# Optimization experiments

Hardware: AMD Instinct MI355X
Metric: run time of the kernel (lower is better)

## Reference

```python
import jax, jax.numpy as jnp
import numpy as np

B, T, V = 32, 100, 20000
E, H, M, DD = 128, 128, 64, 2


def setup_inputs() -> dict:
    key = jax.random.key(0)
    ks = jax.random.split(key, 12)
    x = jax.random.uniform(ks[0], (B, T, V), dtype=jnp.float32)
    # zero out trailing timesteps per example so Masking layer matters
    lens = jax.random.randint(ks[1], (B,), T * 3 // 4, T + 1)
    tmask = (jnp.arange(T)[None, :] < lens[:, None]).astype(jnp.float32)
    x = x * tmask[:, :, None]
    a = jax.random.uniform(ks[2], (B, V), dtype=jnp.float32)
    d = jax.random.normal(ks[3], (B, DD), dtype=jnp.float32)
    # parameters
    emb = jax.random.uniform(ks[4], (V, E), minval=-0.1, maxval=0.1, dtype=jnp.float32)
    s = 1.0 / np.sqrt(E)
    gru_k = jax.random.uniform(ks[5], (E, 3 * H), minval=-s, maxval=s, dtype=jnp.float32)
    gru_rk = jax.random.normal(ks[6], (H, 3 * H), dtype=jnp.float32) / np.sqrt(H)
    gru_b_i = jnp.zeros((3 * H,), jnp.float32)   # input bias (reset_after=True)
    gru_b_r = jnp.zeros((3 * H,), jnp.float32)   # recurrent bias
    s1 = 1.0 / np.sqrt(H + E)
    W1 = jax.random.uniform(ks[7], (H + E, M), minval=-s1, maxval=s1, dtype=jnp.float32)
    b1 = jnp.zeros((M,), jnp.float32)
    s2 = 1.0 / np.sqrt(M + DD)
    W2 = jax.random.uniform(ks[8], (M + DD, 1), minval=-s2, maxval=s2, dtype=jnp.float32)
    b2 = jnp.zeros((1,), jnp.float32)
    return dict(x=x, a=a, d=d, emb=emb, gru_k=gru_k, gru_rk=gru_rk,
                gru_b_i=gru_b_i, gru_b_r=gru_b_r, W1=W1, b1=b1, W2=W2, b2=b2)


def _gru_final_state(xe, mask, gru_k, gru_rk, gru_b_i, gru_b_r):
    # xe: [B,T,E], mask: [B,T] bool. Keras GRU, reset_after=True, eval mode (dropout off).
    Hn = gru_rk.shape[0]
    x_proj = jnp.einsum('bte,eh->bth', xe, gru_k) + gru_b_i  # [B,T,3H]

    def step(h, inp):
        xp_t, m_t = inp                      # [B,3H], [B]
        rec = h @ gru_rk + gru_b_r           # [B,3H]
        xz, xr, xh = jnp.split(xp_t, 3, axis=-1)
        rz, rr, rh = jnp.split(rec, 3, axis=-1)
        z = jax.nn.sigmoid(xz + rz)
        r = jax.nn.sigmoid(xr + rr)
        hh = jnp.tanh(xh + r * rh)
        h_new = z * h + (1.0 - z) * hh
        h = jnp.where(m_t[:, None], h_new, h)  # masked steps carry state
        return h, None

    h0 = jnp.zeros((xe.shape[0], Hn), xe.dtype)
    h_final, _ = jax.lax.scan(step, h0, (jnp.swapaxes(x_proj, 0, 1), jnp.swapaxes(mask, 0, 1)))
    return h_final


def reference(x, a, d, emb, gru_k, gru_rk, gru_b_i, gru_b_r, W1, b1, W2, b2):
    ae = jnp.tanh(a @ emb)                       # [B,E]
    xe = jnp.tanh(jnp.einsum('btv,ve->bte', x, emb))  # [B,T,E]
    mask = jnp.any(xe != 0.0, axis=-1)           # Masking(mask_value=0.0)
    h = _gru_final_state(xe, mask, gru_k, gru_rk, gru_b_i, gru_b_r)  # [B,H]
    c = jnp.tanh(jnp.concatenate([h, ae], axis=1) @ W1 + b1)         # [B,M]
    out = jax.nn.sigmoid(jnp.concatenate([c, d], axis=1) @ W2 + b2)  # [B,1]
    return out
```

## Files before the change

### kernel.cpp

```cpp
#include <hip/hip_runtime.h>

typedef __attribute__((ext_vector_type(8))) short short8;
typedef __attribute__((ext_vector_type(4))) float float4v;

#define V_ 20000

__device__ __forceinline__ unsigned short f2bf(float f) {
    union { float f; unsigned int u; } v; v.f = f;
    unsigned int u = v.u;
    u += 0x7fffu + ((u >> 16) & 1u);
    return (unsigned short)(u >> 16);
}

__device__ __forceinline__ float fast_tanh(float x) {
    float xc = fminf(15.f, fmaxf(-15.f, x));
    float e = __expf(2.f * xc);
    return (e - 1.f) / (e + 1.f);
}

__device__ __forceinline__ float sigmoidf_(float x) {
    float xc = fminf(30.f, fmaxf(-30.f, x));
    return 1.f / (1.f + __expf(-xc));
}

#define GLL16(gp, lp) __builtin_amdgcn_global_load_lds( \
    (const __attribute__((address_space(1))) void*)(gp), \
    (__attribute__((address_space(3))) void*)(lp), 16, 0, 0)

__global__ __launch_bounds__(256) void cvt_embT(const float* __restrict__ emb,
                                                unsigned short* __restrict__ embT) {
    __shared__ unsigned short tile[128 * 65];
    int tid = threadIdx.x;
    int k0 = blockIdx.x * 64;
    const float4v* e4 = (const float4v*)emb;
    #pragma unroll
    for (int c = 0; c < 8; ++c) {
        int l4 = c * 256 + tid;
        int k = l4 >> 5;
        int n4 = l4 & 31;
        float4v f = {0.f, 0.f, 0.f, 0.f};
        if (k0 + k < V_) f = e4[(size_t)(k0 + k) * 32 + n4];
        tile[(n4 * 4 + 0) * 65 + k] = f2bf(f.x);
        tile[(n4 * 4 + 1) * 65 + k] = f2bf(f.y);
        tile[(n4 * 4 + 2) * 65 + k] = f2bf(f.z);
        tile[(n4 * 4 + 3) * 65 + k] = f2bf(f.w);
    }
    __syncthreads();
    #pragma unroll
    for (int c = 0; c < 4; ++c) {
        int l8 = c * 256 + tid;
        int n = l8 >> 3, seg = l8 & 7;
        int kk = k0 + seg * 8;
        if (kk < V_) {
            short8 v;
            #pragma unroll
            for (int i = 0; i < 8; ++i) v[i] = (short)tile[n * 65 + seg * 8 + i];
            *(short8*)(embT + (size_t)n * V_ + kk) = v;
        }
    }
}

__global__ __launch_bounds__(256, 4) void big_gemm(const float* __restrict__ x,
                                                   const float* __restrict__ a,
                                                   const unsigned short* __restrict__ embT,
                                                   float* __restrict__ partial,
                                                   int ks) {
    __shared__ unsigned short Alds[2][128 * 40];
    __shared__ unsigned short Blds[2][128 * 32];
    int tid = threadIdx.x;
    int bx = blockIdx.x, by = blockIdx.y;
    int m0 = bx * 128;
    int per = 625 / ks, extra = 625 % ks;
    int kb0 = by * per + (by < extra ? by : extra);
    int nkb = per + (by < extra ? 1 : 0);

    int lane = tid & 63, wave = tid >> 6;
    int wr = wave >> 1, wc = wave & 1;
    int ln = lane & 15, quad = lane >> 4;

    float4v acc[4][4];
    #pragma unroll
    for (int i = 0; i < 4; ++i)
        #pragma unroll
        for (int j = 0; j < 4; ++j) acc[i][j] = (float4v){0.f, 0.f, 0.f, 0.f};

    int row = tid >> 1, seg = tid & 1;
    int rg = m0 + row;
    int aidx = rg - 3200; aidx = aidx < 0 ? 0 : (aidx > 31 ? 31 : aidx);
    const float* __restrict__ srcA = (rg < 3200) ? (x + (size_t)rg * V_)
                                                 : (a + (size_t)aidx * V_);
    int brow0 = tid >> 2, bkq = tid & 3;
    int wbase = tid & ~63;
    const unsigned short* gB0 = embT + (size_t)brow0 * V_ + bkq * 8;
    const unsigned short* gB1 = embT + (size_t)(64 + brow0) * V_ + bkq * 8;

    float4v fa0, fa1, fa2, fa3;

    {
        int k0 = kb0 * 32;
        const float4v* ap = (const float4v*)(srcA + k0 + seg * 16);
        fa0 = ap[0]; fa1 = ap[1]; fa2 = ap[2]; fa3 = ap[3];
        GLL16(gB0 + k0, &Blds[0][(size_t)wbase * 8]);
        GLL16(gB1 + k0, &Blds[0][(size_t)(256 + wbase) * 8]);
        short8 w0, w1;
        w0[0]=(short)f2bf(fa0.x); w0[1]=(short)f2bf(fa0.y); w0[2]=(short)f2bf(fa0.z); w0[3]=(short)f2bf(fa0.w);
        w0[4]=(short)f2bf(fa1.x); w0[5]=(short)f2bf(fa1.y); w0[6]=(short)f2bf(fa1.z); w0[7]=(short)f2bf(fa1.w);
        w1[0]=(short)f2bf(fa2.x); w1[1]=(short)f2bf(fa2.y); w1[2]=(short)f2bf(fa2.z); w1[3]=(short)f2bf(fa2.w);
        w1[4]=(short)f2bf(fa3.x); w1[5]=(short)f2bf(fa3.y); w1[6]=(short)f2bf(fa3.z); w1[7]=(short)f2bf(fa3.w);
        *(short8*)&Alds[0][row * 40 + seg * 16]     = w0;
        *(short8*)&Alds[0][row * 40 + seg * 16 + 8] = w1;
    }
    __syncthreads();

    for (int it = 0; it < nkb; ++it) {
        int buf = it & 1, nxt = buf ^ 1;
        bool more = (it + 1 < nkb);
        if (more) {
            int k0 = (kb0 + it + 1) * 32;
            const float4v* ap = (const float4v*)(srcA + k0 + seg * 16);
            fa0 = ap[0]; fa1 = ap[1]; fa2 = ap[2]; fa3 = ap[3];
            GLL16(gB0 + k0, &Blds[nxt][(size_t)wbase * 8]);
            GLL16(gB1 + k0, &Blds[nxt][(size_t)(256 + wbase) * 8]);
        }
        short8 af[4];
        #pragma unroll
        for (int i = 0; i < 4; ++i)
            af[i] = *(const short8*)&Alds[buf][(wr * 64 + i * 16 + ln) * 40 + quad * 8];
        #pragma unroll
        for (int j = 0; j < 4; ++j) {
            short8 bf = *(const short8*)&Blds[buf][(wc * 64 + j * 16 + ln) * 32 + quad * 8];
            #pragma unroll
            for (int i = 0; i < 4; ++i)
                acc[i][j] = __builtin_amdgcn_mfma_f32_16x16x32_bf16(af[i], bf, acc[i][j], 0, 0, 0);
        }
        if (more) {
            short8 w0, w1;
            w0[0]=(short)f2bf(fa0.x); w0[1]=(short)f2bf(fa0.y); w0[2]=(short)f2bf(fa0.z); w0[3]=(short)f2bf(fa0.w);
            w0[4]=(short)f2bf(fa1.x); w0[5]=(short)f2bf(fa1.y); w0[6]=(short)f2bf(fa1.z); w0[7]=(short)f2bf(fa1.w);
            w1[0]=(short)f2bf(fa2.x); w1[1]=(short)f2bf(fa2.y); w1[2]=(short)f2bf(fa2.z); w1[3]=(short)f2bf(fa2.w);
            w1[4]=(short)f2bf(fa3.x); w1[5]=(short)f2bf(fa3.y); w1[6]=(short)f2bf(fa3.z); w1[7]=(short)f2bf(fa3.w);
            *(short8*)&Alds[nxt][row * 40 + seg * 16]     = w0;
            *(short8*)&Alds[nxt][row * 40 + seg * 16 + 8] = w1;
        }
        __syncthreads();
    }

    float* dst = partial + (size_t)by * 3328 * 128;
    #pragma unroll
    for (int i = 0; i < 4; ++i) {
        #pragma unroll
        for (int j = 0; j < 4; ++j) {
            int rowb = m0 + wr * 64 + i * 16 + quad * 4;
            int col = wc * 64 + j * 16 + ln;
            #pragma unroll
            for (int r = 0; r < 4; ++r)
                dst[(size_t)(rowb + r) * 128 + col] = acc[i][j][r];
        }
    }
}

__global__ __launch_bounds__(384) void xproj_fused(const float* __restrict__ partial,
                                                   const float* __restrict__ gru_k,
                                                   const float* __restrict__ b_i,
                                                   float* __restrict__ xproj,
                                                   float* __restrict__ maskg,
                                                   float* __restrict__ ae,
                                                   int ks) {
    const size_t SL = (size_t)3328 * 128;
    int tid = threadIdx.x;
    if (blockIdx.x == 200) {
        for (int i = tid; i < 32 * 128; i += 384) {
            float s = 0.f;
            for (int k = 0; k < ks; ++k) s += partial[(size_t)k * SL + 3200 * 128 + i];
            ae[i] = fast_tanh(s);
        }
        return;
    }
    __shared__ float xs[16 * 128];
    __shared__ int anyr[16];
    int row0 = blockIdx.x * 16;
    if (tid < 16) anyr[tid] = 0;
    __syncthreads();
    const float4v* p4 = (const float4v*)partial + (size_t)row0 * 32;
    const size_t SL4 = SL / 4;
    for (int i4 = tid; i4 < 512; i4 += 384) {
        float4v s = p4[i4];
        for (int k = 1; k < ks; ++k) {
            float4v t = p4[(size_t)k * SL4 + i4];
            s.x += t.x; s.y += t.y; s.z += t.z; s.w += t.w;
        }
        float4v v;
        v.x = fast_tanh(s.x); v.y = fast_tanh(s.y);
        v.z = fast_tanh(s.z); v.w = fast_tanh(s.w);
        *(float4v*)&xs[i4 * 4] = v;
        if (v.x != 0.f || v.y != 0.f || v.z != 0.f || v.w != 0.f)
            anyr[i4 >> 5] = 1;
    }
    __syncthreads();
    if (tid < 16) maskg[row0 + tid] = anyr[tid] ? 1.f : 0.f;

    int j = tid;
    float acc[16];
    #pragma unroll
    for (int r = 0; r < 16; ++r) acc[r] = 0.f;
    float bi = b_i[j];
    for (int k4 = 0; k4 < 32; ++k4) {
        float g0 = gru_k[(k4 * 4 + 0) * 384 + j];
        float g1 = gru_k[(k4 * 4 + 1) * 384 + j];
        float g2 = gru_k[(k4 * 4 + 2) * 384 + j];
        float g3 = gru_k[(k4 * 4 + 3) * 384 + j];
        #pragma unroll
        for (int r = 0; r < 16; ++r) {
            float4v xv = *(const float4v*)&xs[r * 128 + k4 * 4];
            acc[r] = fmaf(xv.x, g0, acc[r]);
            acc[r] = fmaf(xv.y, g1, acc[r]);
            acc[r] = fmaf(xv.z, g2, acc[r]);
            acc[r] = fmaf(xv.w, g3, acc[r]);
        }
    }
    #pragma unroll
    for (int r = 0; r < 16; ++r)
        xproj[(size_t)(row0 + r) * 384 + j] = acc[r] + bi;
}

__global__ __launch_bounds__(384) void gru_fused(const float* __restrict__ xproj,
                                                 const float* __restrict__ maskg,
                                                 const float* __restrict__ gru_rk,
                                                 const float* __restrict__ b_r,
                                                 const float* __restrict__ ae,
                                                 const float* __restrict__ d,
                                                 const float* __restrict__ W1,
                                                 const float* __restrict__ b1,
                                                 const float* __restrict__ W2,
                                                 const float* __restrict__ b2,
                                                 float* __restrict__ out) {
    int b = blockIdx.x;
    int j = threadIdx.x;
    float w[128];
    #pragma unroll
    for (int k = 0; k < 128; ++k) w[k] = gru_rk[k * 384 + j];
    float br = b_r[j];
    __shared__ float4v hs4[32];
    __shared__ float recs[384];
    float* hs = (float*)hs4;
    float hreg = 0.f;
    if (j < 128) hs[j] = 0.f;
    const float* xp_base = xproj + (size_t)b * 100 * 384;
    const float* mk = maskg + b * 100;
    float xz = 0.f, xr = 0.f, xh = 0.f;
    if (j < 128) { xz = xp_base[j]; xr = xp_base[128 + j]; xh = xp_base[256 + j]; }
    __syncthreads();
    for (int t = 0; t < 100; ++t) {
        float nxz = 0.f, nxr = 0.f, nxh = 0.f;
        if (t < 99 && j < 128) {
            const float* nb = xp_base + (t + 1) * 384;
            nxz = nb[j]; nxr = nb[128 + j]; nxh = nb[256 + j];
        }
        float s0 = 0.f, s1 = 0.f, s2 = 0.f, s3 = 0.f;
        #pragma unroll
        for (int k4 = 0; k4 < 32; ++k4) {
            float4v hv = hs4[k4];
            s0 = fmaf(hv.x, w[k4 * 4 + 0], s0);
            s1 = fmaf(hv.y, w[k4 * 4 + 1], s1);
            s2 = fmaf(hv.z, w[k4 * 4 + 2], s2);
            s3 = fmaf(hv.w, w[k4 * 4 + 3], s3);
        }
        recs[j] = br + ((s0 + s1) + (s2 + s3));
        __syncthreads();
        if (j < 128) {
            float z = sigmoidf_(xz + recs[j]);
            float r = sigmoidf_(xr + recs[128 + j]);
            float hh = fast_tanh(xh + r * recs[256 + j]);
            float hn = z * hreg + (1.f - z) * hh;
            hreg = (mk[t] != 0.f) ? hn : hreg;
            hs[j] = hreg;
        }
        __syncthreads();
        xz = nxz; xr = nxr; xh = nxh;
    }
    if (j < 64) {
        int m = j;
        float s = b1[m];
        const float* ab = ae + b * 128;
        #pragma unroll 4
        for (int k = 0; k < 128; ++k) s = fmaf(hs[k], W1[k * 64 + m], s);
        #pragma unroll 4
        for (int k = 0; k < 128; ++k) s = fmaf(ab[k], W1[(128 + k) * 64 + m], s);
        float c = fast_tanh(s);
        float p = c * W2[m];
        #pragma unroll
        for (int off = 32; off > 0; off >>= 1) p += __shfl_down(p, off);
        if (m == 0) {
            p += d[b * 2 + 0] * W2[64] + d[b * 2 + 1] * W2[65] + b2[0];
            out[b] = sigmoidf_(p);
        }
    }
}

extern "C" void kernel_launch(void* const* d_in, const int* in_sizes, int n_in,
                              void* d_out, int out_size, void* d_ws, size_t ws_size,
                              hipStream_t stream) {
    (void)in_sizes; (void)n_in; (void)out_size;
    const float* x      = (const float*)d_in[0];
    const float* a      = (const float*)d_in[1];
    const float* d      = (const float*)d_in[2];
    const float* emb    = (const float*)d_in[3];
    const float* gru_k  = (const float*)d_in[4];
    const float* gru_rk = (const float*)d_in[5];
    const float* gbi    = (const float*)d_in[6];
    const float* gbr    = (const float*)d_in[7];
    const float* W1     = (const float*)d_in[8];
    const float* b1     = (const float*)d_in[9];
    const float* W2     = (const float*)d_in[10];
    const float* b2     = (const float*)d_in[11];
    float* out = (float*)d_out;

    char* ws = (char*)d_ws;
    unsigned short* embT = (unsigned short*)(ws);
    const size_t slice = (size_t)3328 * 128 * 4;
    float* partial = (float*)(ws + 5120000);

    int ks = 16;
    {
        size_t fixed_rest = 16384 + 12800 + 4915200;
        while (ks > 1 && 5120000 + (size_t)ks * slice + fixed_rest > ws_size) ks >>= 1;
    }
    char* after = ws + 5120000 + (size_t)ks * slice;
    float* ae      = (float*)(after);
    float* maskg   = (float*)(after + 16384);
    float* xproj   = (float*)(after + 29184);

    hipLaunchKernelGGL(cvt_embT,    dim3(313),    dim3(256), 0, stream, emb, embT);
    hipLaunchKernelGGL(big_gemm,    dim3(26, ks), dim3(256), 0, stream, x, a, embT, partial, ks);
    hipLaunchKernelGGL(xproj_fused, dim3(201),    dim3(384), 0, stream, partial, gru_k, gbi, xproj, maskg, ae, ks);
    hipLaunchKernelGGL(gru_fused,   dim3(32),     dim3(384), 0, stream, xproj, maskg, gru_rk, gbr,
                       ae, d, W1, b1, W2, b2, out);
}
```

Before: 564.9 us.

## Use packed FP32 FMA in projection and GRU, skip trailing masked steps

Rewrites the input-projection and recurrent matvec inner loops to use 2-wide float vectors with elementwise FMA, so the compiler can emit packed FP32 FMA instructions (v_pk_fma_f32) and halve the instruction count. The GRU kernel also computes the last valid timestep per batch from the mask with a shared atomicMax and runs the recurrence only up to that point. Trailing masked steps only carry state, so skipping them is exact, but interior masked steps are still executed. The packed form changes the accumulation order slightly.

```diff
diff --git a/kernel.cpp b/kernel.cpp
--- a/kernel.cpp
+++ b/kernel.cpp
@@ -2,6 +2,7 @@
 
 typedef __attribute__((ext_vector_type(8))) short short8;
 typedef __attribute__((ext_vector_type(4))) float float4v;
+typedef __attribute__((ext_vector_type(2))) float float2v;
 
 #define V_ 20000
 
@@ -200,27 +201,24 @@
     if (tid < 16) maskg[row0 + tid] = anyr[tid] ? 1.f : 0.f;
 
     int j = tid;
-    float acc[16];
-    #pragma unroll
-    for (int r = 0; r < 16; ++r) acc[r] = 0.f;
+    float2v acc[16];
+    #pragma unroll
+    for (int r = 0; r < 16; ++r) acc[r] = (float2v){0.f, 0.f};
     float bi = b_i[j];
     for (int k4 = 0; k4 < 32; ++k4) {
-        float g0 = gru_k[(k4 * 4 + 0) * 384 + j];
-        float g1 = gru_k[(k4 * 4 + 1) * 384 + j];
-        float g2 = gru_k[(k4 * 4 + 2) * 384 + j];
-        float g3 = gru_k[(k4 * 4 + 3) * 384 + j];
+        float2v g01 = { gru_k[(k4 * 4 + 0) * 384 + j], gru_k[(k4 * 4 + 1) * 384 + j] };
+        float2v g23 = { gru_k[(k4 * 4 + 2) * 384 + j], gru_k[(k4 * 4 + 3) * 384 + j] };
         #pragma unroll
         for (int r = 0; r < 16; ++r) {
             float4v xv = *(const float4v*)&xs[r * 128 + k4 * 4];
-            acc[r] = fmaf(xv.x, g0, acc[r]);
-            acc[r] = fmaf(xv.y, g1, acc[r]);
-            acc[r] = fmaf(xv.z, g2, acc[r]);
-            acc[r] = fmaf(xv.w, g3, acc[r]);
+            float2v x01 = {xv.x, xv.y}, x23 = {xv.z, xv.w};
+            acc[r] = __builtin_elementwise_fma(x01, g01, acc[r]);
+            acc[r] = __builtin_elementwise_fma(x23, g23, acc[r]);
         }
     }
     #pragma unroll
     for (int r = 0; r < 16; ++r)
-        xproj[(size_t)(row0 + r) * 384 + j] = acc[r] + bi;
+        xproj[(size_t)(row0 + r) * 384 + j] = (acc[r].x + acc[r].y) + bi;
 }
 
 __global__ __launch_bounds__(384) void gru_fused(const float* __restrict__ xproj,
@@ -236,36 +234,45 @@
                                                  float* __restrict__ out) {
     int b = blockIdx.x;
     int j = threadIdx.x;
-    float w[128];
-    #pragma unroll
-    for (int k = 0; k < 128; ++k) w[k] = gru_rk[k * 384 + j];
+    float2v wv[64];
+    #pragma unroll
+    for (int i = 0; i < 64; ++i) {
+        wv[i] = (float2v){ gru_rk[(2 * i) * 384 + j], gru_rk[(2 * i + 1) * 384 + j] };
+    }
     float br = b_r[j];
     __shared__ float4v hs4[32];
     __shared__ float recs[384];
+    __shared__ int ntS;
     float* hs = (float*)hs4;
     float hreg = 0.f;
+    if (j == 0) ntS = 0;
     if (j < 128) hs[j] = 0.f;
     const float* xp_base = xproj + (size_t)b * 100 * 384;
     const float* mk = maskg + b * 100;
     float xz = 0.f, xr = 0.f, xh = 0.f;
     if (j < 128) { xz = xp_base[j]; xr = xp_base[128 + j]; xh = xp_base[256 + j]; }
     __syncthreads();
-    for (int t = 0; t < 100; ++t) {
+    if (j < 100 && mk[j] != 0.f) atomicMax(&ntS, j + 1);
+    __syncthreads();
+    int nt = ntS;
+    for (int t = 0; t < nt; ++t) {
         float nxz = 0.f, nxr = 0.f, nxh = 0.f;
-        if (t < 99 && j < 128) {
+        if (t + 1 < nt && j < 128) {
             const float* nb = xp_base + (t + 1) * 384;
             nxz = nb[j]; nxr = nb[128 + j]; nxh = nb[256 + j];
         }
-        float s0 = 0.f, s1 = 0.f, s2 = 0.f, s3 = 0.f;
-        #pragma unroll
-        for (int k4 = 0; k4 < 32; ++k4) {
-            float4v hv = hs4[k4];
-            s0 = fmaf(hv.x, w[k4 * 4 + 0], s0);
-            s1 = fmaf(hv.y, w[k4 * 4 + 1], s1);
-            s2 = fmaf(hv.z, w[k4 * 4 + 2], s2);
-            s3 = fmaf(hv.w, w[k4 * 4 + 3], s3);
-        }
-        recs[j] = br + ((s0 + s1) + (s2 + s3));
+        float2v a0 = {0.f, 0.f}, a1 = {0.f, 0.f}, a2 = {0.f, 0.f}, a3 = {0.f, 0.f};
+        #pragma unroll
+        for (int k4 = 0; k4 < 32; k4 += 2) {
+            float4v hA = hs4[k4], hB = hs4[k4 + 1];
+            float2v hA0 = {hA.x, hA.y}, hA1 = {hA.z, hA.w};
+            float2v hB0 = {hB.x, hB.y}, hB1 = {hB.z, hB.w};
+            a0 = __builtin_elementwise_fma(hA0, wv[2 * k4 + 0], a0);
+            a1 = __builtin_elementwise_fma(hA1, wv[2 * k4 + 1], a1);
+            a2 = __builtin_elementwise_fma(hB0, wv[2 * k4 + 2], a2);
+            a3 = __builtin_elementwise_fma(hB1, wv[2 * k4 + 3], a3);
+        }
+        recs[j] = br + (((a0.x + a0.y) + (a1.x + a1.y)) + ((a2.x + a2.y) + (a3.x + a3.y)));
         __syncthreads();
         if (j < 128) {
             float z = sigmoidf_(xz + recs[j]);
```

Result: faster. 543.3 us (-3.8%).
